# Performance work log

Hardware: AMD Instinct MI355X
Metric: run time of the kernel (lower is better)

The kernel has to match this reference:

```python
import jax, jax.numpy as jnp
import numpy as np

B, T, TB, TV, TR = 4, 512, 512, 512, 256
D, H = 1024, 16
HD = D // H
D4 = D // 4
DFF = 4096
ROPE_THETA = 10000.0


def _rms(x, w, eps=1e-6):
    return x * jax.lax.rsqrt(jnp.mean(x * x, -1, keepdims=True) + eps) * w


def _ln(x, w, b, eps=1e-5):
    m = jnp.mean(x, -1, keepdims=True)
    v = jnp.var(x, -1, keepdims=True)
    return (x - m) * jax.lax.rsqrt(v + eps) * w + b


def _rope_cs(L, hd):
    inv = 1.0 / (ROPE_THETA ** (jnp.arange(0, hd, 2, dtype=jnp.float32) / hd))
    f = jnp.arange(L, dtype=jnp.float32)[:, None] * inv[None, :]
    e = jnp.concatenate([f, f], -1)  # (L, hd)
    return jnp.cos(e), jnp.sin(e)


def _rot_half(x):
    h = x.shape[-1] // 2
    return jnp.concatenate([-x[..., h:], x[..., :h]], -1)


def _rope(x, cos, sin):
    return x * cos + _rot_half(x) * sin


def _heads(x):
    b, l, _ = x.shape
    return x.reshape(b, l, H, HD).transpose(0, 2, 1, 3)  # (B,H,L,hd)


def setup_inputs() -> dict:
    key = jax.random.key(0)
    ks = jax.random.split(key, 16)
    def n(k, shape, s=0.02):
        return jax.random.normal(k, shape, jnp.float32) * s
    return {
        'x': n(ks[0], (B, T, D), 1.0),
        'bev_tokens': n(ks[1], (B, TB, D), 1.0),
        'vl_tokens': n(ks[2], (B, TV, D), 1.0),
        'reasoning_tokens': n(ks[3], (B, TR, D), 1.0),
        'conditioning': n(ks[4], (B, D), 1.0),
        'ln_pre_w': jnp.ones((D,)), 'ln_pre_b': jnp.zeros((D,)),
        'adaln_w': n(ks[5], (6 * D, D)), 'adaln_b': jnp.zeros((6 * D,)),
        'q_proj_w': n(ks[6], (D, D)), 'q_proj_b': jnp.zeros((D,)),
        'qa_w': n(ks[7], (3, D4, D)), 'qa_b': jnp.zeros((3, D4)),
        'qa_out_w': n(ks[8], (D, D4)), 'qa_out_b': jnp.zeros((D,)),
        'k_w': n(ks[9], (4, D, D)), 'k_b': jnp.zeros((4, D)),
        'v_w': n(ks[10], (4, D, D)), 'v_b': jnp.zeros((4, D)),
        'o_w': n(ks[11], (D, D)), 'o_b': jnp.zeros((D,)),
        'qn_w': jnp.ones((HD,)), 'kn_w': jnp.ones((HD,)),
        'gating': jnp.full((1,), 0.5, jnp.float32),
        'temps': jnp.zeros((4,)), 'score_biases': jnp.zeros((4,)),
        'ffn_ln_w': jnp.ones((D,)), 'ffn_ln_b': jnp.zeros((D,)),
        'ffn_w1': n(ks[12], (DFF, D)), 'ffn_b1': jnp.zeros((DFF,)),
        'ffn_w2': n(ks[13], (D, DFF)), 'ffn_b2': jnp.zeros((D,)),
    }


def reference(x, bev_tokens, vl_tokens, reasoning_tokens, conditioning,
              ln_pre_w, ln_pre_b, adaln_w, adaln_b,
              q_proj_w, q_proj_b, qa_w, qa_b, qa_out_w, qa_out_b,
              k_w, k_b, v_w, v_b, o_w, o_b, qn_w, kn_w,
              gating, temps, score_biases,
              ffn_ln_w, ffn_ln_b, ffn_w1, ffn_b1, ffn_w2, ffn_b2):
    # AdaLN modulation (T_route == 0 path: single modulation for whole sequence)
    mod = jax.nn.silu(conditioning) @ adaln_w.T + adaln_b  # (B, 6D)
    shift_pre, scale_pre, gate_attn, shift_ffn, scale_ffn, gate_ffn = jnp.split(mod, 6, axis=1)
    x_norm = _ln(x, ln_pre_w, ln_pre_b) * (1.0 + scale_pre[:, None, :]) + shift_pre[:, None, :]

    # Self Q and per-source K/V (sources: self, bev, vl, reasoning)
    q_self = _heads(x_norm @ q_proj_w.T + q_proj_b)
    srcs = [x_norm, bev_tokens, vl_tokens, reasoning_tokens]
    k_all = [_heads(s @ k_w[i].T + k_b[i]) for i, s in enumerate(srcs)]
    v_all = [_heads(s @ v_w[i].T + v_b[i]) for i, s in enumerate(srcs)]

    # Source-specific adapter queries: d -> d/4 -> d (shared out proj)
    q_ad = [_heads((x_norm @ qa_w[i].T + qa_b[i]) @ qa_out_w.T + qa_out_b) for i in range(3)]

    # QK-Norm (RMSNorm on head_dim)
    q_all = [_rms(q, qn_w) for q in [q_self] + q_ad]
    k_all = [_rms(k, kn_w) for k in k_all]

    # RoPE: Q and K for self-attention; K only for cross sources
    cosT, sinT = _rope_cs(x.shape[1], HD)
    q_all[0] = _rope(q_all[0], cosT, sinT)
    k_roped = []
    for k in k_all:
        c, s = _rope_cs(k.shape[2], HD)
        k_roped.append(_rope(k, c, s))

    # Per-source temperature / bias; gating only on reasoning scores
    temp = 1.0 + jax.nn.softplus(temps)
    ratio_g = jnp.tanh(gating[0])
    inv_sqrt_d = HD ** -0.5
    scores = []
    for i in range(4):
        s = jnp.einsum('bhqd,bhkd->bhqk', q_all[i], k_roped[i]) * (inv_sqrt_d * temp[i]) + score_biases[i]
        if i == 3:
            s = s * ratio_g
        scores.append(s)

    attn = jax.nn.softmax(jnp.concatenate(scores, -1), axis=-1)  # joint softmax
    v_cat = jnp.concatenate(v_all, 2)  # (B,H,T+TB+TV+TR,hd)
    out = jnp.einsum('bhqk,bhkd->bhqd', attn, v_cat)
    out = out.transpose(0, 2, 1, 3).reshape(x.shape) @ o_w.T + o_b
    x = x + gate_attn[:, None, :] * out

    # FFN with AdaLN modulation (dropout = identity at eval)
    h = _ln(x, ffn_ln_w, ffn_ln_b) * (1.0 + scale_ffn[:, None, :]) + shift_ffn[:, None, :]
    h = jax.nn.gelu(h @ ffn_w1.T + ffn_b1, approximate=False) @ ffn_w2.T + ffn_b2
    return x + gate_ffn[:, None, :] * h
```

## Files before the change

### kernel.cpp

```cpp
#include <hip/hip_runtime.h>

typedef unsigned short ushort_t;
typedef __attribute__((ext_vector_type(8))) __bf16 bf16x8;
typedef __attribute__((ext_vector_type(4))) float f32x4;

__device__ __forceinline__ float bf2f(ushort_t u) {
    union { unsigned int i; float f; } v; v.i = ((unsigned int)u) << 16; return v.f;
}
__device__ __forceinline__ ushort_t f2bf(float f) {
    union { float f; unsigned int i; } v; v.f = f;
    unsigned int r = (v.i + 0x7FFFu + ((v.i >> 16) & 1u)) >> 16;
    return (ushort_t)r;
}
__device__ __forceinline__ float gelu_exact(float v) {
    return 0.5f * v * (1.f + erff(v * 0.70710678118654752f));
}
__device__ __forceinline__ float ld1(const void* p, size_t i, int isf32) {
    return isf32 ? ((const float*)p)[i] : bf2f(((const ushort_t*)p)[i]);
}
__device__ __forceinline__ void stage8(const void* p, size_t idx, int isf32, ushort_t* dst) {
    if (isf32) {
        const float* f = (const float*)p + idx;
        float4 u = *(const float4*)f;
        float4 v = *(const float4*)(f + 4);
        dst[0] = f2bf(u.x); dst[1] = f2bf(u.y); dst[2] = f2bf(u.z); dst[3] = f2bf(u.w);
        dst[4] = f2bf(v.x); dst[5] = f2bf(v.y); dst[6] = f2bf(v.z); dst[7] = f2bf(v.w);
    } else {
        *(uint4*)dst = *(const uint4*)((const ushort_t*)p + idx);
    }
}
__device__ __forceinline__ void gload16(const ushort_t* g, ushort_t* l) {
    __builtin_amdgcn_global_load_lds(
        (const __attribute__((address_space(1))) unsigned int*)g,
        (__attribute__((address_space(3))) unsigned int*)l, 16, 0, 0);
}

__device__ __forceinline__ void store_q(ushort_t* qbuf, int row, int c, int p0, float v) {
    int b = row >> 9, t = row & 511;
    qbuf[((((size_t)(b * 16 + (c >> 6))) * 4 + p0) * 512 + t) * 64 + (c & 63)] = f2bf(v);
}
__device__ __forceinline__ void store_k(ushort_t* kbuf, int row, int c, int koff, int p1, float v) {
    int b = row >> p1, t = row & ((1 << p1) - 1);
    kbuf[(((size_t)(b * 16 + (c >> 6))) * 1792 + koff + t) * 64 + (c & 63)] = f2bf(v);
}
__device__ __forceinline__ void store_v(ushort_t* vbufT, int row, int c, int koff, int p1, float v) {
    int b = row >> p1, t = row & ((1 << p1) - 1);
    vbufT[(((size_t)(b * 16 + (c >> 6))) * 64 + (c & 63)) * 1792 + koff + t] = f2bf(v);
}

__global__ void detect_kernel(const unsigned int* __restrict__ x, int* __restrict__ flag) {
    if (threadIdx.x == 0 && blockIdx.x == 0) {
        int sane = 0;
        for (int i = 0; i < 256; i++) {
            unsigned int e = (x[i] >> 7) & 0xFFu;
            if (e == 0u || (e >= 100u && e <= 140u)) sane++;
        }
        *flag = (sane >= 200) ? 0 : 1;
    }
}

static constexpr size_t CW_QPROJ = 0;
static constexpr size_t CW_QA    = 1048576;
static constexpr size_t CW_QAOUT = 1835008;
static constexpr size_t CW_KW    = 2097152;
static constexpr size_t CW_VW    = 6291456;
static constexpr size_t CW_OW    = 10485760;
static constexpr size_t CW_FFN1  = 11534336;
static constexpr size_t CW_FFN2  = 15728640;
static constexpr size_t CW_TOTAL = 19922944;

__global__ void __launch_bounds__(256) convert_weights_kernel(
    const void* s0, const void* s1, const void* s2, const void* s3,
    const void* s4, const void* s5, const void* s6, const void* s7,
    ushort_t* __restrict__ dst, const int* __restrict__ dflag) {
    int isf32 = *dflag;
    size_t i8 = ((size_t)blockIdx.x * 256 + threadIdx.x) * 8;
    if (i8 >= CW_TOTAL) return;
    const void* src; size_t base;
    if      (i8 < CW_QA)    { src = s0; base = CW_QPROJ; }
    else if (i8 < CW_QAOUT) { src = s1; base = CW_QA; }
    else if (i8 < CW_KW)    { src = s2; base = CW_QAOUT; }
    else if (i8 < CW_VW)    { src = s3; base = CW_KW; }
    else if (i8 < CW_OW)    { src = s4; base = CW_VW; }
    else if (i8 < CW_FFN1)  { src = s5; base = CW_OW; }
    else if (i8 < CW_FFN2)  { src = s6; base = CW_FFN1; }
    else                    { src = s7; base = CW_FFN2; }
    ushort_t t8[8];
    stage8(src, i8 - base, isf32, t8);
    *(uint4*)(dst + i8) = *(uint4*)t8;
}

__global__ void __launch_bounds__(256) convert_act3_kernel(
    const void* __restrict__ bev, const void* __restrict__ vl,
    const void* __restrict__ reas, ushort_t* __restrict__ actA,
    ushort_t* __restrict__ actB, const int* __restrict__ dflag) {
    int isf32 = *dflag;
    size_t i8 = ((size_t)blockIdx.x * 256 + threadIdx.x) * 8;
    if (i8 >= 5242880) return;
    ushort_t t8[8];
    if (i8 < 2097152) {
        stage8(bev, i8, isf32, t8);
        *(uint4*)(actA + i8) = *(uint4*)t8;
    } else if (i8 < 4194304) {
        stage8(vl, i8 - 2097152, isf32, t8);
        *(uint4*)(actA + i8) = *(uint4*)t8;
    } else {
        stage8(reas, i8 - 4194304, isf32, t8);
        *(uint4*)(actB + (i8 - 4194304)) = *(uint4*)t8;
    }
}

__global__ void prep_consts_kernel(const void* __restrict__ temps,
                                   const void* __restrict__ biases,
                                   const void* __restrict__ gating,
                                   float* __restrict__ consts,
                                   const int* __restrict__ dflag) {
    if (threadIdx.x == 0 && blockIdx.x == 0) {
        int isf32 = *dflag;
        float g = tanhf(ld1(gating, 0, isf32));
        for (int s = 0; s < 4; s++) {
            float t  = ld1(temps, s, isf32);
            float sp = (t > 20.f) ? t : log1pf(expf(t));
            float scale = 0.125f * (1.f + sp);
            float mul = (s == 3) ? g : 1.f;
            consts[s]     = scale * mul;
            consts[4 + s] = ld1(biases, s, isf32) * mul;
        }
    }
}

__global__ void __launch_bounds__(256) adaln_kernel(
    const void* __restrict__ cond, const void* __restrict__ w,
    const void* __restrict__ bias, float* __restrict__ mod,
    int wmode, const int* __restrict__ dflag) {
    __shared__ float cs[1024];
    int isf32 = *dflag;
    int wf = (wmode == 2) ? 0 : isf32;
    int b = blockIdx.y, tid = threadIdx.x;
    for (int i = tid; i < 1024; i += 256) {
        float c = ld1(cond, b * 1024 + i, isf32);
        cs[i] = c / (1.f + expf(-c));
    }
    __syncthreads();
    int n = blockIdx.x * 256 + tid;
    float acc = 0.f;
    if (wf) {
        const float* wr = (const float*)w + (size_t)n * 1024;
        for (int d = 0; d < 1024; d += 8) {
            float4 a = *(const float4*)(wr + d);
            float4 bb = *(const float4*)(wr + d + 4);
            acc += cs[d+0]*a.x + cs[d+1]*a.y + cs[d+2]*a.z + cs[d+3]*a.w
                 + cs[d+4]*bb.x + cs[d+5]*bb.y + cs[d+6]*bb.z + cs[d+7]*bb.w;
        }
    } else {
        const ushort_t* wr = (const ushort_t*)w + (size_t)n * 1024;
        for (int d = 0; d < 1024; d += 8) {
            uint4 raw = *(const uint4*)(wr + d);
            const ushort_t* u = (const ushort_t*)&raw;
            acc += cs[d+0]*bf2f(u[0]) + cs[d+1]*bf2f(u[1]) + cs[d+2]*bf2f(u[2]) + cs[d+3]*bf2f(u[3])
                 + cs[d+4]*bf2f(u[4]) + cs[d+5]*bf2f(u[5]) + cs[d+6]*bf2f(u[6]) + cs[d+7]*bf2f(u[7]);
        }
    }
    mod[(size_t)b * 6144 + n] = acc + ld1(bias, n, isf32);
}

template <int SRC>
__global__ void __launch_bounds__(256) ln_mod_kernel(
    const void* __restrict__ xin, const float* __restrict__ mod,
    const void* __restrict__ lnw, const void* __restrict__ lnb,
    int shift_off, int scale_off, ushort_t* __restrict__ out,
    const int* __restrict__ dflag) {
    int isf32 = *dflag;
    int row = blockIdx.x, tid = threadIdx.x;
    int b = row >> 9;
    float v[4];
    #pragma unroll
    for (int i = 0; i < 4; i++) {
        size_t idx = (size_t)row * 1024 + tid + 256 * i;
        v[i] = (SRC == 1) ? ((const float*)xin)[idx] : ld1(xin, idx, isf32);
    }
    float s = v[0] + v[1] + v[2] + v[3];
    float ss = v[0]*v[0] + v[1]*v[1] + v[2]*v[2] + v[3]*v[3];
    #pragma unroll
    for (int off = 1; off < 64; off <<= 1) {
        s  += __shfl_xor(s,  off, 64);
        ss += __shfl_xor(ss, off, 64);
    }
    __shared__ float red[8];
    int w = tid >> 6;
    if ((tid & 63) == 0) { red[w] = s; red[4 + w] = ss; }
    __syncthreads();
    s  = red[0] + red[1] + red[2] + red[3];
    ss = red[4] + red[5] + red[6] + red[7];
    float mean = s * (1.f / 1024.f);
    float var  = ss * (1.f / 1024.f) - mean * mean;
    float inv  = rsqrtf(var + 1e-5f);
    const float* mb = mod + (size_t)b * 6144;
    #pragma unroll
    for (int i = 0; i < 4; i++) {
        int d = tid + 256 * i;
        float xn = (v[i] - mean) * inv;
        float y  = xn * ld1(lnw, d, isf32) + ld1(lnb, d, isf32);
        out[(size_t)row * 1024 + d] = f2bf(y * (1.f + mb[scale_off + d]) + mb[shift_off + d]);
    }
}

template <int EPI>
__global__ void __launch_bounds__(256) gemm_bt_kernel(
    const void* __restrict__ A, int lda,
    const void* __restrict__ W, int wrow0,
    const void* __restrict__ bias,
    void* __restrict__ Cout, int ldc, int K, int p0, int p1,
    int a_ext, int wmode, const int* __restrict__ dflag) {
    __shared__ ushort_t As[64][40];
    __shared__ ushort_t Bs[64][40];
    int isf32 = *dflag;
    int fa = a_ext ? isf32 : 0;
    int fw = (wmode == 2) ? 0 : isf32;
    int m0 = blockIdx.x * 64, n0 = blockIdx.y * 64;
    int tid = threadIdx.x;
    int r = tid >> 2, c = (tid & 3) * 8;
    int w = tid >> 6, ln = tid & 63;
    int msub = (w & 1) * 32, nsub = (w >> 1) * 32;
    int fr = ln & 15, q = ln >> 4;
    f32x4 acc00 = {0.f,0.f,0.f,0.f}, acc01 = {0.f,0.f,0.f,0.f};
    f32x4 acc10 = {0.f,0.f,0.f,0.f}, acc11 = {0.f,0.f,0.f,0.f};
    for (int k0 = 0; k0 < K; k0 += 32) {
        __syncthreads();
        {
            ushort_t t8[8];
            stage8(A, (size_t)(m0 + r) * lda + c + k0, fa, t8);
            *(uint4*)&As[r][c] = *(uint4*)t8;
        }
        {
            ushort_t t8[8];
            stage8(W, (size_t)(wrow0 + n0 + r) * K + c + k0, fw, t8);
            *(uint4*)&Bs[r][c] = *(uint4*)t8;
        }
        __syncthreads();
        bf16x8 a0 = *(const bf16x8*)&As[msub + fr][q * 8];
        bf16x8 a1 = *(const bf16x8*)&As[msub + 16 + fr][q * 8];
        bf16x8 b0 = *(const bf16x8*)&Bs[nsub + fr][q * 8];
        bf16x8 b1 = *(const bf16x8*)&Bs[nsub + 16 + fr][q * 8];
        acc00 = __builtin_amdgcn_mfma_f32_16x16x32_bf16(a0, b0, acc00, 0, 0, 0);
        acc01 = __builtin_amdgcn_mfma_f32_16x16x32_bf16(a0, b1, acc01, 0, 0, 0);
        acc10 = __builtin_amdgcn_mfma_f32_16x16x32_bf16(a1, b0, acc10, 0, 0, 0);
        acc11 = __builtin_amdgcn_mfma_f32_16x16x32_bf16(a1, b1, acc11, 0, 0, 0);
    }
    int col0 = n0 + nsub + fr;
    float bv0 = ld1(bias, wrow0 + col0, isf32);
    float bv1 = ld1(bias, wrow0 + col0 + 16, isf32);
    #pragma unroll
    for (int mi = 0; mi < 2; mi++) {
        #pragma unroll
        for (int ni = 0; ni < 2; ni++) {
            f32x4 a = (mi == 0) ? (ni == 0 ? acc00 : acc01) : (ni == 0 ? acc10 : acc11);
            int col = col0 + ni * 16;
            float bb = (ni == 0) ? bv0 : bv1;
            #pragma unroll
            for (int e = 0; e < 4; e++) {
                int rowg = m0 + msub + mi * 16 + q * 4 + e;
                float v = a[e] + bb;
                if (EPI == 2) v = gelu_exact(v);
                if (EPI == 0) {
                    ((float*)Cout)[(size_t)rowg * ldc + col] = v;
                } else if (EPI == 1 || EPI == 2) {
                    ((ushort_t*)Cout)[(size_t)rowg * ldc + col] = f2bf(v);
                } else if (EPI == 3) {
                    store_k((ushort_t*)Cout, rowg, col, p0, p1, v);
                } else if (EPI == 5) {
                    store_v((ushort_t*)Cout, rowg, col, p0, p1, v);
                } else {
                    store_q((ushort_t*)Cout, rowg, col, p0, v);
                }
            }
        }
    }
}

__device__ __forceinline__ void gemm_mainloop(
    const ushort_t* __restrict__ A, int lda,
    const ushort_t* __restrict__ W, int ldw,
    int m0, int wrow0, int kbeg, int klen,
    ushort_t* As, ushort_t* Bs, f32x4 acc[4][4])
{
    const int tid = threadIdx.x;
    const int w = tid >> 6;
    const int ln = tid & 63;
    const int fr = ln & 15, q = ln >> 4;
    const int wm = w & 1, wn = w >> 1;
    const ushort_t* gA = A + (size_t)(m0 + (tid >> 2)) * lda + kbeg + (tid & 3) * 8;
    const ushort_t* gW = W + (size_t)(wrow0 + (tid >> 2)) * ldw + kbeg + (tid & 3) * 8;
    const size_t sA = (size_t)64 * lda;
    const size_t sW = (size_t)64 * ldw;
    ushort_t* lA = As + w * 512;
    ushort_t* lB = Bs + w * 512;
    for (int k = 0; k < klen; k += 32) {
        __syncthreads();
        gload16(gA, lA);
        gload16(gA + sA, lA + 2048);
        gload16(gW, lB);
        gload16(gW + sW, lB + 2048);
        gA += 32; gW += 32;
        __syncthreads();
        bf16x8 af[4], bfr[4];
        #pragma unroll
        for (int mi = 0; mi < 4; mi++)
            af[mi] = *(const bf16x8*)&As[(wm * 64 + mi * 16 + fr) * 32 + q * 8];
        #pragma unroll
        for (int ni = 0; ni < 4; ni++)
            bfr[ni] = *(const bf16x8*)&Bs[(wn * 64 + ni * 16 + fr) * 32 + q * 8];
        #pragma unroll
        for (int mi = 0; mi < 4; mi++)
            #pragma unroll
            for (int ni = 0; ni < 4; ni++)
                acc[mi][ni] = __builtin_amdgcn_mfma_f32_16x16x32_bf16(af[mi], bfr[ni], acc[mi][ni], 0, 0, 0);
    }
}

__global__ void __launch_bounds__(256) gemm_stage1_kernel(
    const ushort_t* __restrict__ xnorm,
    const ushort_t* __restrict__ actA, const ushort_t* __restrict__ actB,
    const ushort_t* __restrict__ Wq, const ushort_t* __restrict__ Wqa,
    const ushort_t* __restrict__ Wk, const ushort_t* __restrict__ Wv,
    const void* __restrict__ bq, const void* __restrict__ bqa,
    const void* __restrict__ bk, const void* __restrict__ bv,
    ushort_t* __restrict__ qbuf, ushort_t* __restrict__ qah,
    ushort_t* __restrict__ kbuf, ushort_t* __restrict__ vbufT,
    const int* __restrict__ dflag)
{
    __shared__ ushort_t As[4096], Bs[4096];
    int isf32 = *dflag;
    int bid = blockIdx.x;
    int mode, koff = 0, p1 = 9, srow0, wrow0, am0, boff = 0;
    const ushort_t* A;
    const ushort_t* W;
    const void* bias;
    if (bid < 480) {
        int bx = bid % 16, by = bid / 16;
        am0 = bx * 128; srow0 = am0;
        int n0 = by * 128;
        A = xnorm;
        if (n0 < 1024)      { mode = 0; W = Wq;  bias = bq;  wrow0 = n0; }
        else if (n0 < 1792) { mode = 1; W = Wqa; bias = bqa; wrow0 = n0 - 1024; }
        else if (n0 < 2816) { mode = 2; W = Wk;  bias = bk;  wrow0 = n0 - 1792; }
        else                { mode = 3; W = Wv;  bias = bv;  wrow0 = n0 - 2816; }
    } else {
        int id2 = bid - 480;
        int mb = id2 % 40, ny = id2 / 40;
        int src;
        if (mb < 16)      { src = 0; A = actA; am0 = mb * 128;        srow0 = am0;             koff = 512;  p1 = 9; }
        else if (mb < 32) { src = 1; A = actA; am0 = mb * 128;        srow0 = (mb - 16) * 128; koff = 1024; p1 = 9; }
        else              { src = 2; A = actB; am0 = (mb - 32) * 128; srow0 = am0;             koff = 1536; p1 = 8; }
        int n0 = ny * 128;
        int isK = (n0 < 1024);
        wrow0 = isK ? n0 : n0 - 1024;
        W = (isK ? Wk : Wv) + (size_t)(src + 1) * 1048576;
        bias = isK ? bk : bv;
        boff = (src + 1) * 1024;
        mode = isK ? 2 : 3;
    }
    f32x4 acc[4][4];
    #pragma unroll
    for (int i = 0; i < 4; i++)
        #pragma unroll
        for (int j = 0; j < 4; j++) acc[i][j] = (f32x4){0.f, 0.f, 0.f, 0.f};
    gemm_mainloop(A, 1024, W, 1024, am0, wrow0, 0, 1024, As, Bs, acc);
    int tid = threadIdx.x, w = tid >> 6, ln = tid & 63;
    int fr = ln & 15, q = ln >> 4, wm = w & 1, wn = w >> 1;
    #pragma unroll
    for (int ni = 0; ni < 4; ni++) {
        int c = wrow0 + wn * 64 + ni * 16 + fr;
        float bb = ld1(bias, boff + c, isf32);
        #pragma unroll
        for (int mi = 0; mi < 4; mi++) {
            #pragma unroll
            for (int e = 0; e < 4; e++) {
                int row = srow0 + wm * 64 + mi * 16 + q * 4 + e;
                float v = acc[mi][ni][e] + bb;
                if (mode == 0)      store_q(qbuf, row, c, 0, v);
                else if (mode == 1) qah[(size_t)row * 768 + c] = f2bf(v);
                else if (mode == 2) store_k(kbuf, row, c, koff, p1, v);
                else                store_v(vbufT, row, c, koff, p1, v);
            }
        }
    }
}

__global__ void __launch_bounds__(256) gemm_qaout_kernel(
    const ushort_t* __restrict__ qah,
    const ushort_t* __restrict__ W, const void* __restrict__ bias,
    ushort_t* __restrict__ qbuf, const int* __restrict__ dflag)
{
    __shared__ ushort_t As[4096], Bs[4096];
    int isf32 = *dflag;
    int m0 = blockIdx.x * 128, n0 = blockIdx.y * 128;
    int z = blockIdx.z;
    const ushort_t* A = qah + (size_t)z * 256;
    f32x4 acc[4][4];
    #pragma unroll
    for (int i = 0; i < 4; i++)
        #pragma unroll
        for (int j = 0; j < 4; j++) acc[i][j] = (f32x4){0.f, 0.f, 0.f, 0.f};
    gemm_mainloop(A, 768, W, 256, m0, n0, 0, 256, As, Bs, acc);
    int tid = threadIdx.x, w = tid >> 6, ln = tid & 63;
    int fr = ln & 15, q = ln >> 4, wm = w & 1, wn = w >> 1;
    #pragma unroll
    for (int ni = 0; ni < 4; ni++) {
        int c = n0 + wn * 64 + ni * 16 + fr;
        float bb = ld1(bias, c, isf32);
        #pragma unroll
        for (int mi = 0; mi < 4; mi++) {
            #pragma unroll
            for (int e = 0; e < 4; e++) {
                int row = m0 + wm * 64 + mi * 16 + q * 4 + e;
                store_q(qbuf, row, c, 1 + z, acc[mi][ni][e] + bb);
            }
        }
    }
}

template <int EPI>
__global__ void __launch_bounds__(256) gemm_plain_kernel(
    const ushort_t* __restrict__ A, int lda,
    const ushort_t* __restrict__ W, int ldw,
    const void* __restrict__ bias,
    void* __restrict__ o0, void* __restrict__ o1,
    void* __restrict__ o2, void* __restrict__ o3,
    int ldc, int ksub, const int* __restrict__ dflag)
{
    __shared__ ushort_t As[4096], Bs[4096];
    int isf32 = *dflag;
    int m0 = blockIdx.x * 128, n0 = blockIdx.y * 128;
    int z = blockIdx.z;
    void* Cout = (z == 0) ? o0 : (z == 1) ? o1 : (z == 2) ? o2 : o3;
    f32x4 acc[4][4];
    #pragma unroll
    for (int i = 0; i < 4; i++)
        #pragma unroll
        for (int j = 0; j < 4; j++) acc[i][j] = (f32x4){0.f, 0.f, 0.f, 0.f};
    gemm_mainloop(A, lda, W, ldw, m0, n0, z * ksub, ksub, As, Bs, acc);
    int tid = threadIdx.x, w = tid >> 6, ln = tid & 63;
    int fr = ln & 15, q = ln >> 4, wm = w & 1, wn = w >> 1;
    #pragma unroll
    for (int ni = 0; ni < 4; ni++) {
        int c = n0 + wn * 64 + ni * 16 + fr;
        float bb = (z == 0) ? ld1(bias, c, isf32) : 0.f;
        #pragma unroll
        for (int mi = 0; mi < 4; mi++) {
            #pragma unroll
            for (int e = 0; e < 4; e++) {
                int row = m0 + wm * 64 + mi * 16 + q * 4 + e;
                float v = acc[mi][ni][e] + bb;
                if (EPI == 2) {
                    ((ushort_t*)Cout)[(size_t)row * ldc + c] = f2bf(gelu_exact(v));
                } else {
                    ((float*)Cout)[(size_t)row * ldc + c] = v;
                }
            }
        }
    }
}

__global__ void __launch_bounds__(256) qrope_ip_kernel(
    ushort_t* __restrict__ qbuf, const void* __restrict__ qnw,
    const int* __restrict__ dflag) {
    int isf32 = *dflag;
    int w = threadIdx.x >> 6, ln = threadIdx.x & 63;
    int flat = blockIdx.x * 4 + w;
    int t = flat & 511, s = (flat >> 9) & 3;
    ushort_t* p = qbuf + (size_t)flat * 64;
    float x = bf2f(p[ln]);
    float ssum = x * x;
    #pragma unroll
    for (int off = 1; off < 64; off <<= 1) ssum += __shfl_xor(ssum, off, 64);
    float y = x * rsqrtf(ssum * (1.f / 64.f) + 1e-6f) * ld1(qnw, ln, isf32);
    if (s == 0) {
        float ang = (float)t * __expf(-(float)(ln & 31) * (9.210340371976184f / 32.f));
        float cs, sn;
        sincosf(ang, &sn, &cs);
        float other = __shfl_xor(y, 32, 64);
        y = y * cs + ((ln < 32) ? -other : other) * sn;
    }
    p[ln] = f2bf(y);
}

__global__ void __launch_bounds__(256) krope_ip_kernel(
    ushort_t* __restrict__ kbuf, const void* __restrict__ knw,
    const int* __restrict__ dflag) {
    int isf32 = *dflag;
    int w = threadIdx.x >> 6, ln = threadIdx.x & 63;
    int flat = blockIdx.x * 4 + w;
    int j = flat % 1792;
    int t = j & 511;
    ushort_t* p = kbuf + (size_t)flat * 64;
    float x = bf2f(p[ln]);
    float ssum = x * x;
    #pragma unroll
    for (int off = 1; off < 64; off <<= 1) ssum += __shfl_xor(ssum, off, 64);
    float y = x * rsqrtf(ssum * (1.f / 64.f) + 1e-6f) * ld1(knw, ln, isf32);
    float ang = (float)t * __expf(-(float)(ln & 31) * (9.210340371976184f / 32.f));
    float cs, sn;
    sincosf(ang, &sn, &cs);
    float other = __shfl_xor(y, 32, 64);
    y = y * cs + ((ln < 32) ? -other : other) * sn;
    p[ln] = f2bf(y);
}

__global__ void __launch_bounds__(256) attn_mfma_kernel(
    const ushort_t* __restrict__ qbuf, const ushort_t* __restrict__ kbuf,
    const ushort_t* __restrict__ vbufT, const float* __restrict__ consts,
    float* __restrict__ pacc0, float* __restrict__ pacc1,
    float* __restrict__ pml) {
    __shared__ ushort_t ks[64][72];
    __shared__ ushort_t vsT[64][72];
    __shared__ ushort_t ps[4][16][72];
    int id = blockIdx.x;
    int g  = (id & 7) | ((id >> 6) << 3);
    int qx = (id >> 3) & 7;
    int bh = g & 63;
    int z  = g >> 6;
    int tid = threadIdx.x, w = tid >> 6, ln = tid & 63;
    int r0 = qx * 64 + w * 16;
    int m = ln & 15, quad = ln >> 4;
    const int ntile = z ? 12 : 16;
    const int keybase = z * 1024;
    const int s0i = z * 2;

    const ushort_t* qb = qbuf + (size_t)bh * 4 * 512 * 64;
    bf16x8 qA0f = *(const bf16x8*)(qb + ((size_t)(s0i * 512 + r0 + m)) * 64 + quad * 8);
    bf16x8 qA1f = *(const bf16x8*)(qb + ((size_t)(s0i * 512 + r0 + m)) * 64 + 32 + quad * 8);
    bf16x8 qB0f = *(const bf16x8*)(qb + ((size_t)((s0i + 1) * 512 + r0 + m)) * 64 + quad * 8);
    bf16x8 qB1f = *(const bf16x8*)(qb + ((size_t)((s0i + 1) * 512 + r0 + m)) * 64 + 32 + quad * 8);

    const float aA = consts[s0i],     bA = consts[4 + s0i];
    const float aB = consts[s0i + 1], bB = consts[4 + s0i + 1];

    float m_i[4], l_i[4];
    f32x4 acc[4];
    #pragma unroll
    for (int e = 0; e < 4; e++) { m_i[e] = -1e30f; l_i[e] = 0.f; }
    #pragma unroll
    for (int d = 0; d < 4; d++) acc[d] = (f32x4){0.f, 0.f, 0.f, 0.f};

    const ushort_t* kb  = kbuf  + (size_t)bh * 1792 * 64 + (size_t)keybase * 64;
    const ushort_t* vbT = vbufT + (size_t)bh * 64 * 1792 + keybase;
    int skey = tid >> 3, sd = (tid & 7) * 8;
    uint4 kreg0 = *(const uint4*)(kb + (size_t)skey * 64 + sd);
    uint4 kreg1 = *(const uint4*)(kb + (size_t)(skey + 32) * 64 + sd);
    uint4 vreg0 = *(const uint4*)(vbT + (size_t)skey * 1792 + sd);
    uint4 vreg1 = *(const uint4*)(vbT + (size_t)(skey + 32) * 1792 + sd);
    *(uint4*)&ks[skey][sd]       = kreg0;
    *(uint4*)&ks[skey + 32][sd]  = kreg1;
    *(uint4*)&vsT[skey][sd]      = vreg0;
    *(uint4*)&vsT[skey + 32][sd] = vreg1;
    __syncthreads();

    for (int ti = 0; ti < ntile; ti++) {
        const bool pf = (ti + 1 < ntile);
        if (pf) {
            int nx = (ti + 1) * 64;
            kreg0 = *(const uint4*)(kb + (size_t)(nx + skey) * 64 + sd);
            kreg1 = *(const uint4*)(kb + (size_t)(nx + skey + 32) * 64 + sd);
            vreg0 = *(const uint4*)(vbT + (size_t)skey * 1792 + nx + sd);
            vreg1 = *(const uint4*)(vbT + (size_t)(skey + 32) * 1792 + nx + sd);
        }
        int sl = (ti >= 8) ? 1 : 0;
        float a_s = sl ? aB : aA;
        float b_s = sl ? bB : bA;
        bf16x8 qA0 = sl ? qB0f : qA0f;
        bf16x8 qA1 = sl ? qB1f : qA1f;
        f32x4 zero = {0.f, 0.f, 0.f, 0.f};
        bf16x8 k0a = *(const bf16x8*)&ks[m][quad * 8];
        bf16x8 k0b = *(const bf16x8*)&ks[m][32 + quad * 8];
        bf16x8 k1a = *(const bf16x8*)&ks[16 + m][quad * 8];
        bf16x8 k1b = *(const bf16x8*)&ks[16 + m][32 + quad * 8];
        bf16x8 k2a = *(const bf16x8*)&ks[32 + m][quad * 8];
        bf16x8 k2b = *(const bf16x8*)&ks[32 + m][32 + quad * 8];
        bf16x8 k3a = *(const bf16x8*)&ks[48 + m][quad * 8];
        bf16x8 k3b = *(const bf16x8*)&ks[48 + m][32 + quad * 8];
        f32x4 sc0 = __builtin_amdgcn_mfma_f32_16x16x32_bf16(qA0, k0a, zero, 0, 0, 0);
        sc0 = __builtin_amdgcn_mfma_f32_16x16x32_bf16(qA1, k0b, sc0, 0, 0, 0);
        f32x4 sc1 = __builtin_amdgcn_mfma_f32_16x16x32_bf16(qA0, k1a, zero, 0, 0, 0);
        sc1 = __builtin_amdgcn_mfma_f32_16x16x32_bf16(qA1, k1b, sc1, 0, 0, 0);
        f32x4 sc2 = __builtin_amdgcn_mfma_f32_16x16x32_bf16(qA0, k2a, zero, 0, 0, 0);
        sc2 = __builtin_amdgcn_mfma_f32_16x16x32_bf16(qA1, k2b, sc2, 0, 0, 0);
        f32x4 sc3 = __builtin_amdgcn_mfma_f32_16x16x32_bf16(qA0, k3a, zero, 0, 0, 0);
        sc3 = __builtin_amdgcn_mfma_f32_16x16x32_bf16(qA1, k3b, sc3, 0, 0, 0);
        #pragma unroll
        for (int e = 0; e < 4; e++) {
            float s0 = sc0[e] * a_s + b_s;
            float s1 = sc1[e] * a_s + b_s;
            float s2 = sc2[e] * a_s + b_s;
            float s3 = sc3[e] * a_s + b_s;
            float mxe = fmaxf(fmaxf(s0, s1), fmaxf(s2, s3));
            #pragma unroll
            for (int off = 1; off < 16; off <<= 1) mxe = fmaxf(mxe, __shfl_xor(mxe, off, 64));
            if (mxe > m_i[e] + 8.f) {
                float alpha = __expf(m_i[e] - mxe);
                m_i[e] = mxe;
                l_i[e] *= alpha;
                acc[0][e] *= alpha; acc[1][e] *= alpha;
                acc[2][e] *= alpha; acc[3][e] *= alpha;
            }
            float p0 = __expf(s0 - m_i[e]), p1 = __expf(s1 - m_i[e]);
            float p2 = __expf(s2 - m_i[e]), p3 = __expf(s3 - m_i[e]);
            l_i[e] += (p0 + p1) + (p2 + p3);
            int row = quad * 4 + e;
            ps[w][row][m]      = f2bf(p0);
            ps[w][row][m + 16] = f2bf(p1);
            ps[w][row][m + 32] = f2bf(p2);
            ps[w][row][m + 48] = f2bf(p3);
        }
        bf16x8 pA0 = *(const bf16x8*)&ps[w][m][quad * 8];
        bf16x8 pA1 = *(const bf16x8*)&ps[w][m][32 + quad * 8];
        #pragma unroll
        for (int dsub = 0; dsub < 4; dsub++) {
            bf16x8 vB0 = *(const bf16x8*)&vsT[dsub * 16 + m][quad * 8];
            bf16x8 vB1 = *(const bf16x8*)&vsT[dsub * 16 + m][32 + quad * 8];
            acc[dsub] = __builtin_amdgcn_mfma_f32_16x16x32_bf16(pA0, vB0, acc[dsub], 0, 0, 0);
            acc[dsub] = __builtin_amdgcn_mfma_f32_16x16x32_bf16(pA1, vB1, acc[dsub], 0, 0, 0);
        }
        if (pf) {
            __syncthreads();
            *(uint4*)&ks[skey][sd]       = kreg0;
            *(uint4*)&ks[skey + 32][sd]  = kreg1;
            *(uint4*)&vsT[skey][sd]      = vreg0;
            *(uint4*)&vsT[skey + 32][sd] = vreg1;
            __syncthreads();
        }
    }
    #pragma unroll
    for (int e = 0; e < 4; e++) {
        float l = l_i[e];
        #pragma unroll
        for (int off = 1; off < 16; off <<= 1) l += __shfl_xor(l, off, 64);
        l_i[e] = l;
    }
    float* pacc = z ? pacc1 : pacc0;
    #pragma unroll
    for (int e = 0; e < 4; e++) {
        int t = r0 + quad * 4 + e;
        if (m == 0) {
            size_t mi = (((size_t)z * 64 + bh) * 512 + t) * 2;
            pml[mi]     = m_i[e];
            pml[mi + 1] = l_i[e];
        }
        #pragma unroll
        for (int dsub = 0; dsub < 4; dsub++) {
            pacc[((size_t)bh * 512 + t) * 64 + dsub * 16 + m] = acc[dsub][e];
        }
    }
}

__global__ void __launch_bounds__(256) attn_combine_kernel(
    const float* __restrict__ pacc0, const float* __restrict__ pacc1,
    const float* __restrict__ pml, ushort_t* __restrict__ attn_out) {
    int tid = threadIdx.x, w = tid >> 6, ln = tid & 63;
    int idx = blockIdx.x * 4 + w;
    int bh = idx >> 9, t = idx & 511;
    int b = bh >> 4, h = bh & 15;
    size_t r = (size_t)bh * 512 + t;
    float m0 = pml[r * 2],                 l0 = pml[r * 2 + 1];
    float m1 = pml[((size_t)32768 + r) * 2], l1 = pml[((size_t)32768 + r) * 2 + 1];
    float M = fmaxf(m0, m1);
    float w0 = __expf(m0 - M), w1 = __expf(m1 - M);
    float inv = 1.f / (l0 * w0 + l1 * w1);
    float a0 = pacc0[r * 64 + ln];
    float a1 = pacc1[r * 64 + ln];
    attn_out[(((size_t)(b * 512 + t)) * 16 + h) * 64 + ln] = f2bf((a0 * w0 + a1 * w1) * inv);
}

__global__ void __launch_bounds__(256) attn_mfma_legacy_kernel(
    const ushort_t* __restrict__ qbuf, const ushort_t* __restrict__ kbuf,
    const ushort_t* __restrict__ vbufT, const float* __restrict__ consts,
    ushort_t* __restrict__ attn_out) {
    __shared__ ushort_t ks[2][64][72];
    __shared__ ushort_t vsT[2][64][72];
    __shared__ ushort_t ps[4][16][72];
    int bh = blockIdx.y;
    int b = bh >> 4, h = bh & 15;
    int tid = threadIdx.x, w = tid >> 6, ln = tid & 63;
    int r0 = blockIdx.x * 64 + w * 16;
    int m = ln & 15, quad = ln >> 4;
    const ushort_t* qb = qbuf + (size_t)bh * 4 * 512 * 64;
    bf16x8 qf[4][2];
    #pragma unroll
    for (int s = 0; s < 4; s++) {
        qf[s][0] = *(const bf16x8*)(qb + ((size_t)(s * 512 + r0 + m)) * 64 + quad * 8);
        qf[s][1] = *(const bf16x8*)(qb + ((size_t)(s * 512 + r0 + m)) * 64 + 32 + quad * 8);
    }
    float m_i[4], l_i[4];
    f32x4 acc[4];
    #pragma unroll
    for (int e = 0; e < 4; e++) { m_i[e] = -1e30f; l_i[e] = 0.f; }
    #pragma unroll
    for (int d = 0; d < 4; d++) acc[d] = (f32x4){0.f, 0.f, 0.f, 0.f};
    const ushort_t* kb  = kbuf  + (size_t)bh * 1792 * 64;
    const ushort_t* vbT = vbufT + (size_t)bh * 64 * 1792;
    int skey = tid >> 3, sd = (tid & 7) * 8;
    uint4 kreg0 = *(const uint4*)(kb + (size_t)skey * 64 + sd);
    uint4 kreg1 = *(const uint4*)(kb + (size_t)(skey + 32) * 64 + sd);
    uint4 vreg0 = *(const uint4*)(vbT + (size_t)skey * 1792 + sd);
    uint4 vreg1 = *(const uint4*)(vbT + (size_t)(skey + 32) * 1792 + sd);
    *(uint4*)&ks[0][skey][sd]       = kreg0;
    *(uint4*)&ks[0][skey + 32][sd]  = kreg1;
    *(uint4*)&vsT[0][skey][sd]      = vreg0;
    *(uint4*)&vsT[0][skey + 32][sd] = vreg1;
    __syncthreads();
    int tcnt = 0, p = 0;
    #pragma unroll
    for (int s = 0; s < 4; s++) {
        const float a_s = consts[s];
        const float b_s = consts[4 + s];
        const bf16x8 qA0 = qf[s][0];
        const bf16x8 qA1 = qf[s][1];
        const int NT = (s == 3) ? 4 : 8;
        for (int ti = 0; ti < NT; ti++) {
            if (tcnt < 27) {
                int nx = (tcnt + 1) * 64;
                kreg0 = *(const uint4*)(kb + (size_t)(nx + skey) * 64 + sd);
                kreg1 = *(const uint4*)(kb + (size_t)(nx + skey + 32) * 64 + sd);
                vreg0 = *(const uint4*)(vbT + (size_t)skey * 1792 + nx + sd);
                vreg1 = *(const uint4*)(vbT + (size_t)(skey + 32) * 1792 + nx + sd);
            }
            f32x4 zero = {0.f, 0.f, 0.f, 0.f};
            bf16x8 k0a = *(const bf16x8*)&ks[p][m][quad * 8];
            bf16x8 k0b = *(const bf16x8*)&ks[p][m][32 + quad * 8];
            bf16x8 k1a = *(const bf16x8*)&ks[p][16 + m][quad * 8];
            bf16x8 k1b = *(const bf16x8*)&ks[p][16 + m][32 + quad * 8];
            bf16x8 k2a = *(const bf16x8*)&ks[p][32 + m][quad * 8];
            bf16x8 k2b = *(const bf16x8*)&ks[p][32 + m][32 + quad * 8];
            bf16x8 k3a = *(const bf16x8*)&ks[p][48 + m][quad * 8];
            bf16x8 k3b = *(const bf16x8*)&ks[p][48 + m][32 + quad * 8];
            f32x4 sc0 = __builtin_amdgcn_mfma_f32_16x16x32_bf16(qA0, k0a, zero, 0, 0, 0);
            sc0 = __builtin_amdgcn_mfma_f32_16x16x32_bf16(qA1, k0b, sc0, 0, 0, 0);
            f32x4 sc1 = __builtin_amdgcn_mfma_f32_16x16x32_bf16(qA0, k1a, zero, 0, 0, 0);
            sc1 = __builtin_amdgcn_mfma_f32_16x16x32_bf16(qA1, k1b, sc1, 0, 0, 0);
            f32x4 sc2 = __builtin_amdgcn_mfma_f32_16x16x32_bf16(qA0, k2a, zero, 0, 0, 0);
            sc2 = __builtin_amdgcn_mfma_f32_16x16x32_bf16(qA1, k2b, sc2, 0, 0, 0);
            f32x4 sc3 = __builtin_amdgcn_mfma_f32_16x16x32_bf16(qA0, k3a, zero, 0, 0, 0);
            sc3 = __builtin_amdgcn_mfma_f32_16x16x32_bf16(qA1, k3b, sc3, 0, 0, 0);
            #pragma unroll
            for (int e = 0; e < 4; e++) {
                float s0 = sc0[e] * a_s + b_s;
                float s1 = sc1[e] * a_s + b_s;
                float s2 = sc2[e] * a_s + b_s;
                float s3 = sc3[e] * a_s + b_s;
                float mxe = fmaxf(fmaxf(s0, s1), fmaxf(s2, s3));
                #pragma unroll
                for (int off = 1; off < 16; off <<= 1) mxe = fmaxf(mxe, __shfl_xor(mxe, off, 64));
                if (mxe > m_i[e] + 8.f) {
                    float alpha = __expf(m_i[e] - mxe);
                    m_i[e] = mxe;
                    l_i[e] *= alpha;
                    acc[0][e] *= alpha; acc[1][e] *= alpha;
                    acc[2][e] *= alpha; acc[3][e] *= alpha;
                }
                float p0 = __expf(s0 - m_i[e]), p1 = __expf(s1 - m_i[e]);
                float p2 = __expf(s2 - m_i[e]), p3 = __expf(s3 - m_i[e]);
                l_i[e] += (p0 + p1) + (p2 + p3);
                int row = quad * 4 + e;
                ps[w][row][m]      = f2bf(p0);
                ps[w][row][m + 16] = f2bf(p1);
                ps[w][row][m + 32] = f2bf(p2);
                ps[w][row][m + 48] = f2bf(p3);
            }
            bf16x8 pA0 = *(const bf16x8*)&ps[w][m][quad * 8];
            bf16x8 pA1 = *(const bf16x8*)&ps[w][m][32 + quad * 8];
            #pragma unroll
            for (int dsub = 0; dsub < 4; dsub++) {
                bf16x8 vB0 = *(const bf16x8*)&vsT[p][dsub * 16 + m][quad * 8];
                bf16x8 vB1 = *(const bf16x8*)&vsT[p][dsub * 16 + m][32 + quad * 8];
                acc[dsub] = __builtin_amdgcn_mfma_f32_16x16x32_bf16(pA0, vB0, acc[dsub], 0, 0, 0);
                acc[dsub] = __builtin_amdgcn_mfma_f32_16x16x32_bf16(pA1, vB1, acc[dsub], 0, 0, 0);
            }
            if (tcnt < 27) {
                *(uint4*)&ks[1 - p][skey][sd]       = kreg0;
                *(uint4*)&ks[1 - p][skey + 32][sd]  = kreg1;
                *(uint4*)&vsT[1 - p][skey][sd]      = vreg0;
                *(uint4*)&vsT[1 - p][skey + 32][sd] = vreg1;
            }
            __syncthreads();
            p ^= 1;
            tcnt++;
        }
    }
    #pragma unroll
    for (int e = 0; e < 4; e++) {
        float l = l_i[e];
        #pragma unroll
        for (int off = 1; off < 16; off <<= 1) l += __shfl_xor(l, off, 64);
        float invl = 1.f / l;
        int t = r0 + quad * 4 + e;
        #pragma unroll
        for (int dsub = 0; dsub < 4; dsub++) {
            int d = dsub * 16 + m;
            attn_out[(((size_t)(b * 512 + t)) * 16 + h) * 64 + d] = f2bf(acc[dsub][e] * invl);
        }
    }
}

__global__ void resgate_kernel(const void* __restrict__ x, const float* __restrict__ p0,
                               const float* __restrict__ p1, const float* __restrict__ p2,
                               const float* __restrict__ p3,
                               const float* __restrict__ mod, float* __restrict__ x1,
                               int sum4, const int* __restrict__ dflag) {
    int isf32 = *dflag;
    int i = blockIdx.x * 256 + threadIdx.x;
    int b = i >> 19, n = i & 1023;
    float proj = p0[i];
    if (sum4) proj += p1[i] + p2[i] + p3[i];
    x1[i] = ld1(x, i, isf32) + mod[(size_t)b * 6144 + 2048 + n] * proj;
}
__global__ void final_kernel(const float* __restrict__ x1, const float* __restrict__ f0,
                             const float* __restrict__ f1, const float* __restrict__ f2,
                             const float* __restrict__ f3,
                             const float* __restrict__ mod, void* __restrict__ out,
                             int sum4, const int* __restrict__ dflag) {
    int isf32 = *dflag;
    int i = blockIdx.x * 256 + threadIdx.x;
    int b = i >> 19, n = i & 1023;
    float ffn = f0[i];
    if (sum4) ffn += f1[i] + f2[i] + f3[i];
    float val = x1[i] + mod[(size_t)b * 6144 + 5120 + n] * ffn;
    if (isf32) ((float*)out)[i] = val;
    else       ((ushort_t*)out)[i] = f2bf(val);
}

static constexpr size_t OFF_CONSTS   = 0;
static constexpr size_t OFF_FLAG     = 64;
static constexpr size_t OFF_MOD      = 512;
static constexpr size_t OFF_XNORM    = OFF_MOD    + 98304;
static constexpr size_t OFF_QAH      = OFF_XNORM  + 4194304;
static constexpr size_t OFF_KBUF     = OFF_XNORM  + 8388608;
static constexpr size_t OFF_VBUF     = OFF_KBUF   + 14680064;
static constexpr size_t OFF_QBUF     = OFF_VBUF   + 14680064;
static constexpr size_t OFF_ATTNOUT  = OFF_QBUF   + 16777216;
static constexpr size_t OFF_WCACHE   = OFF_ATTNOUT + 4194304;
static constexpr size_t OFF_PACC1    = OFF_WCACHE + CW_TOTAL * 2;
static constexpr size_t OFF_PML      = OFF_PACC1  + 8388608;
static constexpr size_t WS_NEED      = OFF_WCACHE + 52428800;

extern "C" void kernel_launch(void* const* d_in, const int* in_sizes, int n_in,
                              void* d_out, int out_size, void* d_ws, size_t ws_size,
                              hipStream_t stream) {
    (void)in_sizes; (void)n_in; (void)out_size;
    const void* x        = d_in[0];
    const void* bev      = d_in[1];
    const void* vl       = d_in[2];
    const void* reas     = d_in[3];
    const void* cond     = d_in[4];
    const void* ln_pre_w = d_in[5];
    const void* ln_pre_b = d_in[6];
    const void* adaln_w  = d_in[7];
    const void* adaln_b  = d_in[8];
    const void* q_proj_w = d_in[9];
    const void* q_proj_b = d_in[10];
    const void* qa_w     = d_in[11];
    const void* qa_b     = d_in[12];
    const void* qa_out_w = d_in[13];
    const void* qa_out_b = d_in[14];
    const void* k_w      = d_in[15];
    const void* k_b      = d_in[16];
    const void* v_w      = d_in[17];
    const void* v_b      = d_in[18];
    const void* o_w      = d_in[19];
    const void* o_b      = d_in[20];
    const void* qn_w     = d_in[21];
    const void* kn_w     = d_in[22];
    const void* gating   = d_in[23];
    const void* temps    = d_in[24];
    const void* sbias    = d_in[25];
    const void* ffn_ln_w = d_in[26];
    const void* ffn_ln_b = d_in[27];
    const void* ffn_w1   = d_in[28];
    const void* ffn_b1   = d_in[29];
    const void* ffn_w2   = d_in[30];
    const void* ffn_b2   = d_in[31];

    char* ws = (char*)d_ws;
    float*    consts   = (float*)(ws + OFF_CONSTS);
    int*      dflag    = (int*)(ws + OFF_FLAG);
    float*    mod      = (float*)(ws + OFF_MOD);
    ushort_t* xnorm    = (ushort_t*)(ws + OFF_XNORM);
    ushort_t* qah      = (ushort_t*)(ws + OFF_QAH);
    ushort_t* kbuf     = (ushort_t*)(ws + OFF_KBUF);
    ushort_t* vbufT    = (ushort_t*)(ws + OFF_VBUF);
    ushort_t* qbuf     = (ushort_t*)(ws + OFF_QBUF);
    ushort_t* attnout  = (ushort_t*)(ws + OFF_ATTNOUT);
    float*    x1       = (float*)(ws + OFF_XNORM);
    ushort_t* hmid     = (ushort_t*)(ws + OFF_KBUF);
    ushort_t* hin      = (ushort_t*)(ws + OFF_ATTNOUT);
    ushort_t* wc       = (ushort_t*)(ws + OFF_WCACHE);
    float*    pacc0    = (float*)(ws + OFF_XNORM);
    float*    pacc1    = (float*)(ws + OFF_PACC1);
    float*    pml      = (float*)(ws + OFF_PML);
    ushort_t* actA     = (ushort_t*)(ws + OFF_PACC1);
    ushort_t* actB     = (ushort_t*)(ws + OFF_ATTNOUT);
    float*    op0      = (float*)(ws + OFF_KBUF);
    float*    op1      = (float*)(ws + OFF_KBUF + 8388608);
    float*    op2      = (float*)(ws + OFF_KBUF + 16777216);
    float*    op3      = (float*)(ws + OFF_QBUF);
    float*    f0       = (float*)(ws + OFF_QBUF);
    float*    f1       = (float*)(ws + OFF_QBUF + 8388608);
    float*    f2       = (float*)(ws + OFF_KBUF + 16777216);
    float*    f3       = (float*)(ws + OFF_PACC1);

    const bool use_cache = (ws_size >= WS_NEED);

    detect_kernel<<<1, 64, 0, stream>>>((const unsigned int*)x, dflag);
    prep_consts_kernel<<<1, 64, 0, stream>>>(temps, sbias, gating, consts, dflag);

    if (use_cache) {
        convert_weights_kernel<<<9728, 256, 0, stream>>>(
            q_proj_w, qa_w, qa_out_w, k_w, v_w, o_w, ffn_w1, ffn_w2, wc, dflag);
        convert_act3_kernel<<<2560, 256, 0, stream>>>(bev, vl, reas, actA, actB, dflag);
        adaln_kernel<<<dim3(24, 4), 256, 0, stream>>>(cond, adaln_w, adaln_b, mod, 0, dflag);
        ln_mod_kernel<0><<<2048, 256, 0, stream>>>(x, mod, ln_pre_w, ln_pre_b, 0, 1024, xnorm, dflag);

        gemm_stage1_kernel<<<1120, 256, 0, stream>>>(
            xnorm, actA, actB,
            wc + CW_QPROJ, wc + CW_QA, wc + CW_KW, wc + CW_VW,
            q_proj_b, qa_b, k_b, v_b, qbuf, qah, kbuf, vbufT, dflag);
        gemm_qaout_kernel<<<dim3(16, 8, 3), 256, 0, stream>>>(
            qah, wc + CW_QAOUT, qa_out_b, qbuf, dflag);

        qrope_ip_kernel<<<32768, 256, 0, stream>>>(qbuf, qn_w, dflag);
        krope_ip_kernel<<<28672, 256, 0, stream>>>(kbuf, kn_w, dflag);
        attn_mfma_kernel<<<1024, 256, 0, stream>>>(
            qbuf, kbuf, vbufT, consts, pacc0, pacc1, pml);
        attn_combine_kernel<<<8192, 256, 0, stream>>>(pacc0, pacc1, pml, attnout);

        gemm_plain_kernel<0><<<dim3(16, 8, 4), 256, 0, stream>>>(
            attnout, 1024, wc + CW_OW, 1024, o_b, op0, op1, op2, op3, 1024, 256, dflag);
        resgate_kernel<<<8192, 256, 0, stream>>>(x, op0, op1, op2, op3, mod, x1, 1, dflag);
        ln_mod_kernel<1><<<2048, 256, 0, stream>>>(x1, mod, ffn_ln_w, ffn_ln_b, 3072, 4096, hin, dflag);
        gemm_plain_kernel<2><<<dim3(16, 32, 1), 256, 0, stream>>>(
            hin, 1024, wc + CW_FFN1, 1024, ffn_b1, hmid, nullptr, nullptr, nullptr, 4096, 1024, dflag);
        gemm_plain_kernel<0><<<dim3(16, 8, 4), 256, 0, stream>>>(
            hmid, 4096, wc + CW_FFN2, 4096, ffn_b2, f0, f1, f2, f3, 1024, 1024, dflag);
        final_kernel<<<8192, 256, 0, stream>>>(x1, f0, f1, f2, f3, mod, d_out, 1, dflag);
    } else {
        float* proj0L = (float*)(ws + OFF_QBUF);
        adaln_kernel<<<dim3(24, 4), 256, 0, stream>>>(cond, adaln_w, adaln_b, mod, 0, dflag);
        ln_mod_kernel<0><<<2048, 256, 0, stream>>>(x, mod, ln_pre_w, ln_pre_b, 0, 1024, xnorm, dflag);
        gemm_bt_kernel<4><<<dim3(32, 16), 256, 0, stream>>>(xnorm, 1024, q_proj_w, 0, q_proj_b, qbuf, 0, 1024, 0, 9, 0, 0, dflag);
        {
            const void* srcs[4] = {xnorm, bev, vl, reas};
            const int koffs[4] = {0, 512, 1024, 1536};
            const int p1s[4]   = {9, 9, 9, 8};
            for (int i = 0; i < 4; i++) {
                int aext = (i == 0) ? 0 : 1;
                int gx = (i == 3) ? 16 : 32;
                gemm_bt_kernel<3><<<dim3(gx, 16), 256, 0, stream>>>(
                    srcs[i], 1024, k_w, i * 1024, k_b, kbuf, 0, 1024, koffs[i], p1s[i], aext, 0, dflag);
                gemm_bt_kernel<5><<<dim3(gx, 16), 256, 0, stream>>>(
                    srcs[i], 1024, v_w, i * 1024, v_b, vbufT, 0, 1024, koffs[i], p1s[i], aext, 0, dflag);
            }
        }
        gemm_bt_kernel<1><<<dim3(32, 12), 256, 0, stream>>>(xnorm, 1024, qa_w, 0, qa_b, qah, 768, 1024, 0, 0, 0, 0, dflag);
        for (int i = 0; i < 3; i++)
            gemm_bt_kernel<4><<<dim3(32, 16), 256, 0, stream>>>(qah + i * 256, 768, qa_out_w, 0, qa_out_b,
                                                                qbuf, 0, 256, 1 + i, 9, 0, 0, dflag);
        qrope_ip_kernel<<<32768, 256, 0, stream>>>(qbuf, qn_w, dflag);
        krope_ip_kernel<<<28672, 256, 0, stream>>>(kbuf, kn_w, dflag);
        attn_mfma_legacy_kernel<<<dim3(8, 64), 256, 0, stream>>>(qbuf, kbuf, vbufT, consts, attnout);
        gemm_bt_kernel<0><<<dim3(32, 16), 256, 0, stream>>>(attnout, 1024, o_w, 0, o_b, proj0L, 1024, 1024, 0, 0, 0, 0, dflag);
        resgate_kernel<<<8192, 256, 0, stream>>>(x, proj0L, proj0L, proj0L, proj0L, mod, x1, 0, dflag);
        ln_mod_kernel<1><<<2048, 256, 0, stream>>>(x1, mod, ffn_ln_w, ffn_ln_b, 3072, 4096, hin, dflag);
        gemm_bt_kernel<2><<<dim3(32, 64), 256, 0, stream>>>(hin, 1024, ffn_w1, 0, ffn_b1, hmid, 4096, 1024, 0, 0, 0, 0, dflag);
        gemm_bt_kernel<0><<<dim3(32, 16), 256, 0, stream>>>(hmid, 4096, ffn_w2, 0, ffn_b2, proj0L, 1024, 4096, 0, 0, 0, 0, dflag);
        final_kernel<<<8192, 256, 0, stream>>>(x1, proj0L, proj0L, proj0L, proj0L, mod, d_out, 0, dflag);
    }
}
```

Baseline: 579.1 us.

## Fuse per-head RMSNorm and RoPE into projection GEMM epilogues

Moves the per-head RMS normalization and rotary embedding for Q and K into the epilogues of the stage-1 projection GEMM and the qa_out GEMM, and removes the separate in-place qrope/krope passes over qbuf and kbuf. Each head's 64 columns sit in one wave's 16-lane group, so the sum of squares is reduced with xor shuffles, and RoPE pairs columns d and d+32 held by the same lane. A small cos/sin table is precomputed by a new kernel. This removes two full read-modify-write sweeps of Q and K in exchange for heavier epilogues, higher register pressure, and a table that may differ slightly from the reference rope values.

Result: faster. 526.3 us (-9.1%).

```diff
diff --git a/kernel.cpp b/kernel.cpp
--- a/kernel.cpp
+++ b/kernel.cpp
@@ -57,6 +57,16 @@
         }
         *flag = (sane >= 200) ? 0 : 1;
     }
+}
+
+__global__ void prep_rope_kernel(float* __restrict__ tab) {
+    int idx = blockIdx.x * 256 + threadIdx.x;
+    int t = idx >> 5, d = idx & 31;
+    float ang = (float)t * __expf(-(float)d * (9.210340371976184f / 32.f));
+    float cs, sn;
+    sincosf(ang, &sn, &cs);
+    tab[idx * 2]     = cs;
+    tab[idx * 2 + 1] = sn;
 }
 
 static constexpr size_t CW_QPROJ = 0;
@@ -325,6 +335,8 @@
     const ushort_t* __restrict__ Wk, const ushort_t* __restrict__ Wv,
     const void* __restrict__ bq, const void* __restrict__ bqa,
     const void* __restrict__ bk, const void* __restrict__ bv,
+    const void* __restrict__ qnw, const void* __restrict__ knw,
+    const float* __restrict__ ropetab,
     ushort_t* __restrict__ qbuf, ushort_t* __restrict__ qah,
     ushort_t* __restrict__ kbuf, ushort_t* __restrict__ vbufT,
     const int* __restrict__ dflag)
@@ -367,21 +379,67 @@
         for (int j = 0; j < 4; j++) acc[i][j] = (f32x4){0.f, 0.f, 0.f, 0.f};
     gemm_mainloop(A, 1024, W, 1024, am0, wrow0, 0, 1024, As, Bs, acc);
     int tid = threadIdx.x, w = tid >> 6, ln = tid & 63;
-    int fr = ln & 15, q = ln >> 4, wm = w & 1, wn = w >> 1;
-    #pragma unroll
-    for (int ni = 0; ni < 4; ni++) {
-        int c = wrow0 + wn * 64 + ni * 16 + fr;
-        float bb = ld1(bias, boff + c, isf32);
-        #pragma unroll
-        for (int mi = 0; mi < 4; mi++) {
-            #pragma unroll
-            for (int e = 0; e < 4; e++) {
-                int row = srow0 + wm * 64 + mi * 16 + q * 4 + e;
-                float v = acc[mi][ni][e] + bb;
-                if (mode == 0)      store_q(qbuf, row, c, 0, v);
-                else if (mode == 1) qah[(size_t)row * 768 + c] = f2bf(v);
-                else if (mode == 2) store_k(kbuf, row, c, koff, p1, v);
-                else                store_v(vbufT, row, c, koff, p1, v);
+    int fr = ln & 15, q = tid & 63; q = (ln >> 4);
+    int wm = w & 1, wn = w >> 1;
+    float bb[4], nw[4];
+    #pragma unroll
+    for (int ni = 0; ni < 4; ni++)
+        bb[ni] = ld1(bias, boff + wrow0 + wn * 64 + ni * 16 + fr, isf32);
+    if (mode == 0 || mode == 2) {
+        const void* nwp = (mode == 0) ? qnw : knw;
+        #pragma unroll
+        for (int ni = 0; ni < 4; ni++) nw[ni] = ld1(nwp, ni * 16 + fr, isf32);
+    }
+    const int tmask = (1 << p1) - 1;
+    #pragma unroll
+    for (int mi = 0; mi < 4; mi++) {
+        #pragma unroll
+        for (int e = 0; e < 4; e++) {
+            int row = srow0 + wm * 64 + mi * 16 + q * 4 + e;
+            float v0 = acc[mi][0][e] + bb[0];
+            float v1 = acc[mi][1][e] + bb[1];
+            float v2 = acc[mi][2][e] + bb[2];
+            float v3 = acc[mi][3][e] + bb[3];
+            int c0 = wrow0 + wn * 64 + fr;
+            if (mode == 1) {
+                qah[(size_t)row * 768 + c0]      = f2bf(v0);
+                qah[(size_t)row * 768 + c0 + 16] = f2bf(v1);
+                qah[(size_t)row * 768 + c0 + 32] = f2bf(v2);
+                qah[(size_t)row * 768 + c0 + 48] = f2bf(v3);
+            } else if (mode == 3) {
+                store_v(vbufT, row, c0,      koff, p1, v0);
+                store_v(vbufT, row, c0 + 16, koff, p1, v1);
+                store_v(vbufT, row, c0 + 32, koff, p1, v2);
+                store_v(vbufT, row, c0 + 48, koff, p1, v3);
+            } else {
+                float ss = v0*v0 + v1*v1 + v2*v2 + v3*v3;
+                ss += __shfl_xor(ss, 1, 64);
+                ss += __shfl_xor(ss, 2, 64);
+                ss += __shfl_xor(ss, 4, 64);
+                ss += __shfl_xor(ss, 8, 64);
+                float inv = rsqrtf(ss * (1.f / 64.f) + 1e-6f);
+                float y0 = v0 * inv * nw[0];
+                float y1 = v1 * inv * nw[1];
+                float y2 = v2 * inv * nw[2];
+                float y3 = v3 * inv * nw[3];
+                int t = row & tmask;
+                float2 cs0 = *(const float2*)&ropetab[((t << 5) + fr) * 2];
+                float2 cs1 = *(const float2*)&ropetab[((t << 5) + 16 + fr) * 2];
+                float r0 = y0 * cs0.x - y2 * cs0.y;
+                float r1 = y1 * cs1.x - y3 * cs1.y;
+                float r2 = y2 * cs0.x + y0 * cs0.y;
+                float r3 = y3 * cs1.x + y1 * cs1.y;
+                if (mode == 0) {
+                    store_q(qbuf, row, c0,      0, r0);
+                    store_q(qbuf, row, c0 + 16, 0, r1);
+                    store_q(qbuf, row, c0 + 32, 0, r2);
+                    store_q(qbuf, row, c0 + 48, 0, r3);
+                } else {
+                    store_k(kbuf, row, c0,      koff, p1, r0);
+                    store_k(kbuf, row, c0 + 16, koff, p1, r1);
+                    store_k(kbuf, row, c0 + 32, koff, p1, r2);
+                    store_k(kbuf, row, c0 + 48, koff, p1, r3);
+                }
             }
         }
     }
@@ -390,6 +448,7 @@
 __global__ void __launch_bounds__(256) gemm_qaout_kernel(
     const ushort_t* __restrict__ qah,
     const ushort_t* __restrict__ W, const void* __restrict__ bias,
+    const void* __restrict__ qnw,
     ushort_t* __restrict__ qbuf, const int* __restrict__ dflag)
 {
     __shared__ ushort_t As[4096], Bs[4096];
@@ -405,17 +464,32 @@
     gemm_mainloop(A, 768, W, 256, m0, n0, 0, 256, As, Bs, acc);
     int tid = threadIdx.x, w = tid >> 6, ln = tid & 63;
     int fr = ln & 15, q = ln >> 4, wm = w & 1, wn = w >> 1;
+    float bb[4], nw[4];
     #pragma unroll
     for (int ni = 0; ni < 4; ni++) {
-        int c = n0 + wn * 64 + ni * 16 + fr;
-        float bb = ld1(bias, c, isf32);
-        #pragma unroll
-        for (int mi = 0; mi < 4; mi++) {
-            #pragma unroll
-            for (int e = 0; e < 4; e++) {
-                int row = m0 + wm * 64 + mi * 16 + q * 4 + e;
-                store_q(qbuf, row, c, 1 + z, acc[mi][ni][e] + bb);
-            }
+        bb[ni] = ld1(bias, n0 + wn * 64 + ni * 16 + fr, isf32);
+        nw[ni] = ld1(qnw, ni * 16 + fr, isf32);
+    }
+    #pragma unroll
+    for (int mi = 0; mi < 4; mi++) {
+        #pragma unroll
+        for (int e = 0; e < 4; e++) {
+            int row = m0 + wm * 64 + mi * 16 + q * 4 + e;
+            float v0 = acc[mi][0][e] + bb[0];
+            float v1 = acc[mi][1][e] + bb[1];
+            float v2 = acc[mi][2][e] + bb[2];
+            float v3 = acc[mi][3][e] + bb[3];
+            float ss = v0*v0 + v1*v1 + v2*v2 + v3*v3;
+            ss += __shfl_xor(ss, 1, 64);
+            ss += __shfl_xor(ss, 2, 64);
+            ss += __shfl_xor(ss, 4, 64);
+            ss += __shfl_xor(ss, 8, 64);
+            float inv = rsqrtf(ss * (1.f / 64.f) + 1e-6f);
+            int c0 = n0 + wn * 64 + fr;
+            store_q(qbuf, row, c0,      1 + z, v0 * inv * nw[0]);
+            store_q(qbuf, row, c0 + 16, 1 + z, v1 * inv * nw[1]);
+            store_q(qbuf, row, c0 + 32, 1 + z, v2 * inv * nw[2]);
+            store_q(qbuf, row, c0 + 48, 1 + z, v3 * inv * nw[3]);
         }
     }
 }
@@ -840,6 +914,7 @@
 static constexpr size_t OFF_WCACHE   = OFF_ATTNOUT + 4194304;
 static constexpr size_t OFF_PACC1    = OFF_WCACHE + CW_TOTAL * 2;
 static constexpr size_t OFF_PML      = OFF_PACC1  + 8388608;
+static constexpr size_t OFF_ROPE     = OFF_PML    + 524288;
 static constexpr size_t WS_NEED      = OFF_WCACHE + 52428800;
 
 extern "C" void kernel_launch(void* const* d_in, const int* in_sizes, int n_in,
@@ -893,6 +968,7 @@
     ushort_t* hmid     = (ushort_t*)(ws + OFF_KBUF);
     ushort_t* hin      = (ushort_t*)(ws + OFF_ATTNOUT);
     ushort_t* wc       = (ushort_t*)(ws + OFF_WCACHE);
+    float*    ropetab  = (float*)(ws + OFF_ROPE);
     float*    pacc0    = (float*)(ws + OFF_XNORM);
     float*    pacc1    = (float*)(ws + OFF_PACC1);
     float*    pml      = (float*)(ws + OFF_PML);
@@ -913,6 +989,7 @@
     prep_consts_kernel<<<1, 64, 0, stream>>>(temps, sbias, gating, consts, dflag);
 
     if (use_cache) {
+        prep_rope_kernel<<<64, 256, 0, stream>>>(ropetab);
         convert_weights_kernel<<<9728, 256, 0, stream>>>(
             q_proj_w, qa_w, qa_out_w, k_w, v_w, o_w, ffn_w1, ffn_w2, wc, dflag);
         convert_act3_kernel<<<2560, 256, 0, stream>>>(bev, vl, reas, actA, actB, dflag);
@@ -922,12 +999,11 @@
         gemm_stage1_kernel<<<1120, 256, 0, stream>>>(
             xnorm, actA, actB,
             wc + CW_QPROJ, wc + CW_QA, wc + CW_KW, wc + CW_VW,
-            q_proj_b, qa_b, k_b, v_b, qbuf, qah, kbuf, vbufT, dflag);
+            q_proj_b, qa_b, k_b, v_b, qn_w, kn_w, ropetab,
+            qbuf, qah, kbuf, vbufT, dflag);
         gemm_qaout_kernel<<<dim3(16, 8, 3), 256, 0, stream>>>(
-            qah, wc + CW_QAOUT, qa_out_b, qbuf, dflag);
-
-        qrope_ip_kernel<<<32768, 256, 0, stream>>>(qbuf, qn_w, dflag);
-        krope_ip_kernel<<<28672, 256, 0, stream>>>(kbuf, kn_w, dflag);
+            qah, wc + CW_QAOUT, qa_out_b, qn_w, qbuf, dflag);
+
         attn_mfma_kernel<<<1024, 256, 0, stream>>>(
             qbuf, kbuf, vbufT, consts, pacc0, pacc1, pml);
         attn_combine_kernel<<<8192, 256, 0, stream>>>(pacc0, pacc1, pml, attnout);
```
